# Kernel optimization log

Measured on AMD Instinct MI355X. Metric: run time of the kernel, lower is better.

Reference implementation:

```python
import jax, jax.numpy as jnp
import numpy as np

# Model dims
B, S, H, E, I, K = 2, 2048, 1024, 8, 1024, 2
ALPHA, LIMIT = 1.702, 7.0  # gpt_oss activation constants (module defaults)


def setup_inputs() -> dict:
    key = jax.random.key(0)
    ks = jax.random.split(key, 5)
    sc = 0.02
    return {
        "hidden_states": jax.random.normal(ks[0], (B, S, H), jnp.float32),
        "router_weight": jax.random.normal(ks[1], (H, E), jnp.float32) * sc,
        "gate_up_proj": jax.random.normal(ks[2], (E, H, 2 * I), jnp.float32) * sc,
        "gate_up_proj_bias": jnp.zeros((E, 2 * I), jnp.float32),
        "down_proj": jax.random.normal(ks[3], (E, I, H), jnp.float32) * sc,
        "down_proj_bias": jnp.zeros((E, H), jnp.float32),
    }


def reference(hidden_states, router_weight, gate_up_proj, gate_up_proj_bias,
              down_proj, down_proj_bias):
    Bt, St, Ht = hidden_states.shape
    x = hidden_states.reshape(-1, Ht)           # [T, H], T = B*S
    T = x.shape[0]

    # Router: linear -> top-k -> softmax over selected logits (gpt_oss style)
    logits = x @ router_weight                  # [T, E]
    top_vals, top_idx = jax.lax.top_k(logits, K)
    scores = jax.nn.softmax(top_vals, axis=-1)  # [T, K]
    # Sparse combine weights: w[t, e] = score if e selected for t, else 0
    w = jnp.zeros((T, E), x.dtype).at[jnp.arange(T)[:, None], top_idx].set(scores)

    # Fused gate+up projection for every expert (dense equivalent of grouped GEMM;
    # unselected experts get zero combine weight so math matches sparse path)
    gu = jnp.einsum('th,ehf->tef', x, gate_up_proj) + gate_up_proj_bias  # [T, E, 2I]
    gate = gu[..., ::2]                         # interleaved gate (default)
    up = gu[..., 1::2]
    gate = jnp.minimum(gate, LIMIT)
    up = jnp.clip(up, -LIMIT, LIMIT)
    glu = gate * jax.nn.sigmoid(gate * ALPHA)
    act = (up + 1.0) * glu                      # [T, E, I]

    down = jnp.einsum('tei,eih->teh', act, down_proj) + down_proj_bias  # [T, E, H]

    # Weighted combine over experts (all-to-all combine is identity at D=1)
    out = jnp.einsum('te,teh->th', w, down)     # [T, H]
    return out.reshape(Bt, St, Ht)
```

## Files before the change

kernel.cpp:

```cpp
#include <hip/hip_runtime.h>
#include <hip/hip_bf16.h>
#include <cstdint>
#include <cstddef>

constexpr int T_TOK = 4096;
constexpr int H_DIM = 1024;
constexpr int E_NUM = 8;
constexpr int I_DIM = 1024;
constexpr int F2    = 2048;
constexpr float ALPHA = 1.702f;
constexpr float LIMIT = 7.0f;
constexpr int BM = 128;
constexpr int BK = 32;
constexpr int NT = 32;
constexpr int MAXT = 72;

using u16    = unsigned short;
using bf16x8 = __attribute__((ext_vector_type(8))) __bf16;
using s16x8  = __attribute__((ext_vector_type(8))) short;
using f32x4  = __attribute__((ext_vector_type(4))) float;

constexpr size_t WS_W1T  = 0;
constexpr size_t WS_DOWN = 0;
constexpr size_t WS_W2T  = 33554432;
constexpr size_t WS_ACT  = 50331648;
constexpr size_t WS_ETOK = 67108864;
constexpr size_t WS_POS  = 67239936;
constexpr size_t WS_CNT  = 67272704;
constexpr size_t WS_ROWB = 67272736;
constexpr size_t WS_ASGN = 67272768;
constexpr size_t WS_TOPE = 67273792;
constexpr size_t WS_TOPW = 67290176;
constexpr size_t WS_XBF  = 67322944;
constexpr size_t WS_NEED = 75711552;

__device__ __forceinline__ u16 f2bf(float f) {
    union { float f; unsigned u; } v; v.f = f;
    return (u16)((v.u + 0x7FFFu + ((v.u >> 16) & 1u)) >> 16);
}
__device__ __forceinline__ float bf2f(u16 u) {
    union { unsigned u; float f; } v; v.u = (unsigned)u << 16; return v.f;
}

__device__ __forceinline__ s16x8 pack8(float4 a, float4 b) {
    s16x8 r;
    r[0] = (short)f2bf(a.x); r[1] = (short)f2bf(a.y);
    r[2] = (short)f2bf(a.z); r[3] = (short)f2bf(a.w);
    r[4] = (short)f2bf(b.x); r[5] = (short)f2bf(b.y);
    r[6] = (short)f2bf(b.z); r[7] = (short)f2bf(b.w);
    return r;
}

__device__ __forceinline__ void gload16(const void* g, void* l) {
    __builtin_amdgcn_global_load_lds((const __attribute__((address_space(1))) unsigned*)g,
                                     (__attribute__((address_space(3))) unsigned*)l,
                                     16, 0, 0);
}

__device__ __forceinline__ void pipe_sync() {
    __builtin_amdgcn_sched_barrier(0);
    asm volatile("s_waitcnt vmcnt(0) lgkmcnt(0)" ::: "memory");
    __builtin_amdgcn_s_barrier();
    __builtin_amdgcn_sched_barrier(0);
}

__global__ __launch_bounds__(256) void k_xbf(const float* __restrict__ x,
                                             u16* __restrict__ xbf) {
    const size_t i = ((size_t)blockIdx.x * 256 + threadIdx.x) * 8;
    float4 a = *(const float4*)(x + i);
    float4 b = *(const float4*)(x + i + 4);
    *(s16x8*)(xbf + i) = pack8(a, b);
}

__global__ __launch_bounds__(256) void k_transpose_w1(const float* __restrict__ in,
                                                      u16* __restrict__ out) {
    __shared__ float tile[64][65];
    const int e = blockIdx.z, c0 = blockIdx.x * 64, h0 = blockIdx.y * 64;
    const int tid = threadIdx.x;
    const float* src = in + ((size_t)e * H_DIM + h0) * F2 + c0;
#pragma unroll
    for (int i = 0; i < 4; ++i) {
        int r = (tid >> 4) + i * 16, c = (tid & 15) * 4;
        float4 v = *(const float4*)(src + (size_t)r * F2 + c);
        tile[r][c] = v.x; tile[r][c + 1] = v.y; tile[r][c + 2] = v.z; tile[r][c + 3] = v.w;
    }
    __syncthreads();
    const int c = tid >> 2, hseg = (tid & 3) * 16;
    const int g = c & 1;
    const int f = (c0 + c) >> 1;
    u16* dst = out + (((size_t)e * 2 + g) * I_DIM + f) * H_DIM + h0 + hseg;
    s16x8 o0, o1;
#pragma unroll
    for (int j = 0; j < 8; ++j) o0[j] = (short)f2bf(tile[hseg + j][c]);
#pragma unroll
    for (int j = 0; j < 8; ++j) o1[j] = (short)f2bf(tile[hseg + 8 + j][c]);
    *(s16x8*)dst = o0;
    *(s16x8*)(dst + 8) = o1;
}

__global__ __launch_bounds__(256) void k_transpose_w2(const float* __restrict__ in,
                                                      u16* __restrict__ out) {
    __shared__ float tile[64][65];
    const int e = blockIdx.z, h0 = blockIdx.x * 64, i0 = blockIdx.y * 64;
    const int tid = threadIdx.x;
    const float* src = in + ((size_t)e * I_DIM + i0) * H_DIM + h0;
#pragma unroll
    for (int i = 0; i < 4; ++i) {
        int r = (tid >> 4) + i * 16, c = (tid & 15) * 4;
        float4 v = *(const float4*)(src + (size_t)r * H_DIM + c);
        tile[r][c] = v.x; tile[r][c + 1] = v.y; tile[r][c + 2] = v.z; tile[r][c + 3] = v.w;
    }
    __syncthreads();
    const int c = tid >> 2, iseg = (tid & 3) * 16;
    u16* dst = out + ((size_t)e * H_DIM + h0 + c) * I_DIM + i0 + iseg;
    s16x8 o0, o1;
#pragma unroll
    for (int j = 0; j < 8; ++j) o0[j] = (short)f2bf(tile[iseg + j][c]);
#pragma unroll
    for (int j = 0; j < 8; ++j) o1[j] = (short)f2bf(tile[iseg + 8 + j][c]);
    *(s16x8*)dst = o0;
    *(s16x8*)(dst + 8) = o1;
}

__global__ __launch_bounds__(256) void k_router_top2(const float* __restrict__ x,
                                                     const float* __restrict__ rw,
                                                     int* __restrict__ tope,
                                                     float2* __restrict__ topw) {
    const int wave = threadIdx.x >> 6, lane = threadIdx.x & 63;
    const int t = blockIdx.x * 4 + wave;
    const float* xr = x + (size_t)t * H_DIM;
    float acc[E_NUM];
#pragma unroll
    for (int e = 0; e < E_NUM; ++e) acc[e] = 0.f;
    for (int h = lane; h < H_DIM; h += 64) {
        float xv = xr[h];
        const float* r = rw + h * E_NUM;
#pragma unroll
        for (int e = 0; e < E_NUM; ++e) acc[e] += xv * r[e];
    }
#pragma unroll
    for (int e = 0; e < E_NUM; ++e) {
        float v = acc[e];
#pragma unroll
        for (int o = 32; o > 0; o >>= 1) v += __shfl_down(v, o);
        acc[e] = v;
    }
    if (lane == 0) {
        int e0 = 0; float v0 = acc[0];
#pragma unroll
        for (int e = 1; e < E_NUM; ++e) if (acc[e] > v0) { v0 = acc[e]; e0 = e; }
        int e1 = -1; float v1 = -3.4e38f;
#pragma unroll
        for (int e = 0; e < E_NUM; ++e) if (e != e0 && acc[e] > v1) { v1 = acc[e]; e1 = e; }
        float ew = expf(v1 - v0);
        float inv = 1.f / (1.f + ew);
        tope[t] = e0 | (e1 << 8);
        topw[t] = make_float2(inv, ew * inv);
    }
}

__global__ __launch_bounds__(256) void k_router_scatter(const int* __restrict__ tope,
                                                        int* __restrict__ cnt,
                                                        int* __restrict__ ent_tok,
                                                        int2* __restrict__ pos) {
    __shared__ int lcnt[E_NUM];
    __shared__ int gbase[E_NUM];
    const int tid = threadIdx.x;
    const int t = blockIdx.x * 256 + tid;
    if (tid < E_NUM) lcnt[tid] = 0;
    __syncthreads();
    const int pk = tope[t];
    const int e0 = pk & 0xff, e1 = pk >> 8;
    const int o0 = atomicAdd(&lcnt[e0], 1);
    const int o1 = atomicAdd(&lcnt[e1], 1);
    __syncthreads();
    if (tid < E_NUM) gbase[tid] = atomicAdd(&cnt[tid], lcnt[tid]);
    __syncthreads();
    const int p0 = gbase[e0] + o0;
    const int p1 = gbase[e1] + o1;
    ent_tok[e0 * T_TOK + p0] = t;
    ent_tok[e1 * T_TOK + p1] = t;
    pos[t] = make_int2(p0, p1);
}

__global__ void k_schedule(const int* __restrict__ cnt, int* __restrict__ rowbase,
                           int* __restrict__ assign) {
    if (threadIdx.x == 0) {
        int rb = 0, na = 0;
        for (int e = 0; e < E_NUM; ++e) {
            rowbase[e] = rb;
            int nt = (cnt[e] + BM - 1) >> 7;
            for (int m = 0; m < nt; ++m) assign[na++] = (e << 16) | m;
            rb += cnt[e];
        }
        for (; na < MAXT; ++na) assign[na] = -1;
    }
}

__global__ __launch_bounds__(256, 3) void k_gemm1(
    const u16* __restrict__ xbf, const u16* __restrict__ w1t,
    const float* __restrict__ bias, const int* __restrict__ ent_tok,
    const int* __restrict__ cnt, const int* __restrict__ rowbase,
    const int* __restrict__ assign, u16* __restrict__ act) {
    const int a = assign[blockIdx.y];
    if (a < 0) return;
    const int e = a >> 16, mt = a & 0xffff;
    const int j0 = blockIdx.x * 64;
    const int cs = cnt[e], r0 = mt * BM;
    __shared__ __align__(16) u16 As[2][BM * BK];
    __shared__ __align__(16) u16 Bs[2][BM * BK];
    const int tid = threadIdx.x, lane = tid & 63, wv = tid >> 6;
    const int lr = lane >> 2;
    const int sm = (lane & 3) ^ (lr & 3);
    const u16* asrc[2]; const u16* bsrc[2]; int dofs[2];
#pragma unroll
    for (int j = 0; j < 2; ++j) {
        const int row = wv * 32 + j * 16 + lr;
        const int aent = r0 + row;
        const int tok = (aent < cs) ? ent_tok[e * T_TOK + aent] : 0;
        asrc[j] = xbf + (size_t)tok * H_DIM + sm * 8;
        const int g = row >> 6;
        const int f = j0 + (row & 63);
        bsrc[j] = w1t + (((size_t)e * 2 + g) * I_DIM + f) * H_DIM + sm * 8;
        dofs[j] = (wv * 32 + j * 16) * BK;
    }
    const int wm = wv >> 1, wn = wv & 1;
    const int lcol = lane & 15, lk = lane >> 4;
    int aoff[4], goff[2], uoff[2];
#pragma unroll
    for (int mi = 0; mi < 4; ++mi) {
        const int r = wm * 64 + mi * 16 + lcol;
        aoff[mi] = r * 64 + ((lk ^ (r & 3)) << 4);
    }
#pragma unroll
    for (int nj = 0; nj < 2; ++nj) {
        const int rg_ = wn * 32 + nj * 16 + lcol;
        const int ru  = 64 + rg_;
        goff[nj] = rg_ * 64 + ((lk ^ (rg_ & 3)) << 4);
        uoff[nj] = ru  * 64 + ((lk ^ (ru  & 3)) << 4);
    }
    f32x4 ag[4][2], au[4][2];
    const f32x4 z = {0.f, 0.f, 0.f, 0.f};
#pragma unroll
    for (int mi = 0; mi < 4; ++mi) { ag[mi][0] = z; ag[mi][1] = z; au[mi][0] = z; au[mi][1] = z; }
#pragma unroll
    for (int j = 0; j < 2; ++j) {
        gload16(asrc[j], &As[0][dofs[j]]);
        gload16(bsrc[j], &Bs[0][dofs[j]]);
    }
    pipe_sync();
    int cur = 0;
    for (int t = 0; t < NT; ++t) {
        if (t + 1 < NT) {
            const int kn = (t + 1) * BK;
            u16* Ad = As[cur ^ 1]; u16* Bd = Bs[cur ^ 1];
#pragma unroll
            for (int j = 0; j < 2; ++j) {
                gload16(asrc[j] + kn, Ad + dofs[j]);
                gload16(bsrc[j] + kn, Bd + dofs[j]);
            }
        }
        const char* Ab = (const char*)As[cur];
        const char* Bb = (const char*)Bs[cur];
        bf16x8 af[4];
#pragma unroll
        for (int mi = 0; mi < 4; ++mi) af[mi] = *(const bf16x8*)(Ab + aoff[mi]);
        const bf16x8 g0 = *(const bf16x8*)(Bb + goff[0]);
        const bf16x8 g1 = *(const bf16x8*)(Bb + goff[1]);
        const bf16x8 u0 = *(const bf16x8*)(Bb + uoff[0]);
        const bf16x8 u1 = *(const bf16x8*)(Bb + uoff[1]);
#pragma unroll
        for (int mi = 0; mi < 4; ++mi) {
            ag[mi][0] = __builtin_amdgcn_mfma_f32_16x16x32_bf16(af[mi], g0, ag[mi][0], 0, 0, 0);
            au[mi][0] = __builtin_amdgcn_mfma_f32_16x16x32_bf16(af[mi], u0, au[mi][0], 0, 0, 0);
            ag[mi][1] = __builtin_amdgcn_mfma_f32_16x16x32_bf16(af[mi], g1, ag[mi][1], 0, 0, 0);
            au[mi][1] = __builtin_amdgcn_mfma_f32_16x16x32_bf16(af[mi], u1, au[mi][1], 0, 0, 0);
        }
        pipe_sync();
        cur ^= 1;
    }
    const int rbase = rowbase[e];
#pragma unroll
    for (int mi = 0; mi < 4; ++mi) {
#pragma unroll
        for (int nj = 0; nj < 2; ++nj) {
            const int col = j0 + wn * 32 + nj * 16 + lcol;
            const float bg_ = bias[e * F2 + 2 * col];
            const float bu_ = bias[e * F2 + 2 * col + 1];
#pragma unroll
            for (int rg = 0; rg < 4; ++rg) {
                const int r = wm * 64 + mi * 16 + lk * 4 + rg;
                if (r0 + r < cs) {
                    float gv = ag[mi][nj][rg] + bg_;
                    float uv = au[mi][nj][rg] + bu_;
                    gv = fminf(gv, LIMIT);
                    uv = fminf(fmaxf(uv, -LIMIT), LIMIT);
                    const float glu = gv / (1.f + expf(-ALPHA * gv));
                    act[(size_t)(rbase + r0 + r) * I_DIM + col] = f2bf((uv + 1.f) * glu);
                }
            }
        }
    }
}

__global__ __launch_bounds__(256, 3) void k_gemm2(
    const u16* __restrict__ act, const u16* __restrict__ w2t,
    const int* __restrict__ cnt, const int* __restrict__ rowbase,
    const int* __restrict__ assign, u16* __restrict__ down) {
    const int a = assign[blockIdx.y];
    if (a < 0) return;
    const int e = a >> 16, mt = a & 0xffff;
    const int n0 = blockIdx.x * 128;
    const int cs = cnt[e], r0 = mt * BM, rbase = rowbase[e];
    __shared__ __align__(16) u16 As[2][BM * BK];
    __shared__ __align__(16) u16 Bs[2][BM * BK];
    const int tid = threadIdx.x, lane = tid & 63, wv = tid >> 6;
    const int lr = lane >> 2;
    const int sm = (lane & 3) ^ (lr & 3);
    const u16* asrc[2]; const u16* bsrc[2]; int dofs[2];
#pragma unroll
    for (int j = 0; j < 2; ++j) {
        const int row = wv * 32 + j * 16 + lr;
        int ar = rbase + r0 + row;
        if (ar > 2 * T_TOK - 1) ar = 2 * T_TOK - 1;
        asrc[j] = act + (size_t)ar * I_DIM + sm * 8;
        bsrc[j] = w2t + ((size_t)e * H_DIM + n0 + row) * I_DIM + sm * 8;
        dofs[j] = (wv * 32 + j * 16) * BK;
    }
    const int wm = wv >> 1, wn = wv & 1;
    const int lcol = lane & 15, lk = lane >> 4;
    int aoff[4], boff[4];
#pragma unroll
    for (int mi = 0; mi < 4; ++mi) {
        const int r = wm * 64 + mi * 16 + lcol;
        const int b = wn * 64 + mi * 16 + lcol;
        aoff[mi] = r * 64 + ((lk ^ (r & 3)) << 4);
        boff[mi] = b * 64 + ((lk ^ (b & 3)) << 4);
    }
    f32x4 acc[4][4];
    const f32x4 z = {0.f, 0.f, 0.f, 0.f};
#pragma unroll
    for (int mi = 0; mi < 4; ++mi)
#pragma unroll
        for (int nj = 0; nj < 4; ++nj) acc[mi][nj] = z;
#pragma unroll
    for (int j = 0; j < 2; ++j) {
        gload16(asrc[j], &As[0][dofs[j]]);
        gload16(bsrc[j], &Bs[0][dofs[j]]);
    }
    pipe_sync();
    int cur = 0;
    for (int t = 0; t < NT; ++t) {
        if (t + 1 < NT) {
            const int kn = (t + 1) * BK;
            u16* Ad = As[cur ^ 1]; u16* Bd = Bs[cur ^ 1];
#pragma unroll
            for (int j = 0; j < 2; ++j) {
                gload16(asrc[j] + kn, Ad + dofs[j]);
                gload16(bsrc[j] + kn, Bd + dofs[j]);
            }
        }
        const char* Ab = (const char*)As[cur];
        const char* Bb = (const char*)Bs[cur];
        bf16x8 af[4], bf_[4];
#pragma unroll
        for (int mi = 0; mi < 4; ++mi) af[mi]  = *(const bf16x8*)(Ab + aoff[mi]);
#pragma unroll
        for (int nj = 0; nj < 4; ++nj) bf_[nj] = *(const bf16x8*)(Bb + boff[nj]);
#pragma unroll
        for (int mi = 0; mi < 4; ++mi)
#pragma unroll
            for (int nj = 0; nj < 4; ++nj)
                acc[mi][nj] = __builtin_amdgcn_mfma_f32_16x16x32_bf16(af[mi], bf_[nj], acc[mi][nj], 0, 0, 0);
        pipe_sync();
        cur ^= 1;
    }
#pragma unroll
    for (int mi = 0; mi < 4; ++mi) {
#pragma unroll
        for (int nj = 0; nj < 4; ++nj) {
            const int col = n0 + wn * 64 + nj * 16 + lcol;
#pragma unroll
            for (int rg = 0; rg < 4; ++rg) {
                const int r = wm * 64 + mi * 16 + lk * 4 + rg;
                if (r0 + r < cs)
                    down[(size_t)(rbase + r0 + r) * H_DIM + col] = f2bf(acc[mi][nj][rg]);
            }
        }
    }
}

__global__ __launch_bounds__(256) void k_combine(
    const int* __restrict__ tope, const float2* __restrict__ topw,
    const int2* __restrict__ pos, const int* __restrict__ rowb,
    const float* __restrict__ b2, const u16* __restrict__ down,
    float* __restrict__ out) {
    const int t = blockIdx.x;
    const int c = threadIdx.x * 4;
    const int pk = tope[t];
    const int e0 = pk & 0xff, e1 = pk >> 8;
    const int2 pp = pos[t];
    const float2 w = topw[t];
    const size_t ro0 = (size_t)(rowb[e0] + pp.x) * H_DIM;
    const size_t ro1 = (size_t)(rowb[e1] + pp.y) * H_DIM;
    ushort4 d0 = *(const ushort4*)(down + ro0 + c);
    ushort4 d1 = *(const ushort4*)(down + ro1 + c);
    float4 bb0 = *(const float4*)(b2 + e0 * H_DIM + c);
    float4 bb1 = *(const float4*)(b2 + e1 * H_DIM + c);
    float4 o;
    o.x = w.x * (bf2f(d0.x) + bb0.x) + w.y * (bf2f(d1.x) + bb1.x);
    o.y = w.x * (bf2f(d0.y) + bb0.y) + w.y * (bf2f(d1.y) + bb1.y);
    o.z = w.x * (bf2f(d0.z) + bb0.z) + w.y * (bf2f(d1.z) + bb1.z);
    o.w = w.x * (bf2f(d0.w) + bb0.w) + w.y * (bf2f(d1.w) + bb1.w);
    *(float4*)(out + (size_t)t * H_DIM + c) = o;
}

extern "C" void kernel_launch(void* const* d_in, const int* in_sizes, int n_in,
                              void* d_out, int out_size, void* d_ws, size_t ws_size,
                              hipStream_t stream) {
    const float* x   = (const float*)d_in[0];
    const float* rw  = (const float*)d_in[1];
    const float* w1  = (const float*)d_in[2];
    const float* b1  = (const float*)d_in[3];
    const float* w2  = (const float*)d_in[4];
    const float* b2  = (const float*)d_in[5];
    float* out = (float*)d_out;
    char* ws = (char*)d_ws;

    if (ws_size < WS_NEED) return;

    u16*    W1T  = (u16*)(ws + WS_W1T);
    u16*    DOWN = (u16*)(ws + WS_DOWN);
    u16*    W2T  = (u16*)(ws + WS_W2T);
    u16*    ACT  = (u16*)(ws + WS_ACT);
    int*    ETOK = (int*)(ws + WS_ETOK);
    int2*   POS  = (int2*)(ws + WS_POS);
    int*    CNT  = (int*)(ws + WS_CNT);
    int*    ROWB = (int*)(ws + WS_ROWB);
    int*    ASGN = (int*)(ws + WS_ASGN);
    int*    TOPE = (int*)(ws + WS_TOPE);
    float2* TOPW = (float2*)(ws + WS_TOPW);
    u16*    XBF  = (u16*)(ws + WS_XBF);

    hipMemsetAsync(CNT, 0, E_NUM * sizeof(int), stream);

    k_xbf<<<T_TOK * H_DIM / 2048, 256, 0, stream>>>(x, XBF);
    k_transpose_w1<<<dim3(32, 16, 8), 256, 0, stream>>>(w1, W1T);
    k_transpose_w2<<<dim3(16, 16, 8), 256, 0, stream>>>(w2, W2T);
    k_router_top2<<<T_TOK / 4, 256, 0, stream>>>(x, rw, TOPE, TOPW);
    k_router_scatter<<<T_TOK / 256, 256, 0, stream>>>(TOPE, CNT, ETOK, POS);
    k_schedule<<<1, 64, 0, stream>>>(CNT, ROWB, ASGN);
    k_gemm1<<<dim3(16, MAXT), 256, 0, stream>>>(XBF, W1T, b1, ETOK, CNT, ROWB, ASGN, ACT);
    k_gemm2<<<dim3(8, MAXT), 256, 0, stream>>>(ACT, W2T, CNT, ROWB, ASGN, DOWN);
    k_combine<<<T_TOK, 256, 0, stream>>>(TOPE, TOPW, POS, ROWB, b2, DOWN, out);
}
```

Measured before the change: 166.6 us.

## Restructure MoE GEMMs as persistent 512-thread kernels with triple-buffered 256x64 tiles

Both grouped expert GEMMs become persistent kernels: 256 blocks of 512 threads loop over a job list built from a device-side tile count, replacing the old grid padded with empty tiles. Tiles grow to 256 rows with BK=64 and a three-stage LDS ring, using partial vmcnt waits so loads run two stages ahead of the MFMAs. The LDS swizzle is widened to 8 chunks and s_setprio is raised around the MFMA blocks. The larger tiles and extra LDS buffer reduce occupancy and add more row padding for experts with few tokens.

```diff
diff --git a/kernel.cpp b/kernel.cpp
--- a/kernel.cpp
+++ b/kernel.cpp
@@ -10,10 +10,14 @@
 constexpr int F2    = 2048;
 constexpr float ALPHA = 1.702f;
 constexpr float LIMIT = 7.0f;
-constexpr int BM = 128;
-constexpr int BK = 32;
-constexpr int NT = 32;
-constexpr int MAXT = 72;
+constexpr int BM  = 256;
+constexpr int BK  = 64;
+constexpr int NKT = 16;
+constexpr int BN1 = 64;
+constexpr int NP1 = I_DIM / BN1;
+constexpr int BN2 = 128;
+constexpr int NP2 = H_DIM / BN2;
+constexpr int MAXT = 40;
 
 using u16    = unsigned short;
 using bf16x8 = __attribute__((ext_vector_type(8))) __bf16;
@@ -57,12 +61,9 @@
                                      16, 0, 0);
 }
 
-__device__ __forceinline__ void pipe_sync() {
-    __builtin_amdgcn_sched_barrier(0);
-    asm volatile("s_waitcnt vmcnt(0) lgkmcnt(0)" ::: "memory");
-    __builtin_amdgcn_s_barrier();
-    __builtin_amdgcn_sched_barrier(0);
-}
+#define SB0() __builtin_amdgcn_sched_barrier(0)
+#define BARRIER() do { SB0(); __builtin_amdgcn_s_barrier(); SB0(); } while (0)
+#define WVM(n) asm volatile("s_waitcnt vmcnt(" #n ")" ::: "memory")
 
 __global__ __launch_bounds__(256) void k_xbf(const float* __restrict__ x,
                                              u16* __restrict__ xbf) {
@@ -184,207 +185,252 @@
 }
 
 __global__ void k_schedule(const int* __restrict__ cnt, int* __restrict__ rowbase,
-                           int* __restrict__ assign) {
+                           int* __restrict__ assign, int* __restrict__ ntot) {
     if (threadIdx.x == 0) {
         int rb = 0, na = 0;
         for (int e = 0; e < E_NUM; ++e) {
             rowbase[e] = rb;
-            int nt = (cnt[e] + BM - 1) >> 7;
+            int nt = (cnt[e] + BM - 1) >> 8;
             for (int m = 0; m < nt; ++m) assign[na++] = (e << 16) | m;
             rb += cnt[e];
         }
+        ntot[0] = na;
         for (; na < MAXT; ++na) assign[na] = -1;
     }
 }
 
-__global__ __launch_bounds__(256, 3) void k_gemm1(
+__global__ __launch_bounds__(512, 2) void k_gemm1(
     const u16* __restrict__ xbf, const u16* __restrict__ w1t,
     const float* __restrict__ bias, const int* __restrict__ ent_tok,
     const int* __restrict__ cnt, const int* __restrict__ rowbase,
-    const int* __restrict__ assign, u16* __restrict__ act) {
-    const int a = assign[blockIdx.y];
-    if (a < 0) return;
-    const int e = a >> 16, mt = a & 0xffff;
-    const int j0 = blockIdx.x * 64;
-    const int cs = cnt[e], r0 = mt * BM;
-    __shared__ __align__(16) u16 As[2][BM * BK];
-    __shared__ __align__(16) u16 Bs[2][BM * BK];
+    const int* __restrict__ assign, const int* __restrict__ ntotp,
+    u16* __restrict__ act) {
+    __shared__ __align__(16) u16 As[3][BM * BK];
+    __shared__ __align__(16) u16 Bs[3][128 * BK];
+    const int ntot = ntotp[0];
     const int tid = threadIdx.x, lane = tid & 63, wv = tid >> 6;
-    const int lr = lane >> 2;
-    const int sm = (lane & 3) ^ (lr & 3);
-    const u16* asrc[2]; const u16* bsrc[2]; int dofs[2];
-#pragma unroll
-    for (int j = 0; j < 2; ++j) {
-        const int row = wv * 32 + j * 16 + lr;
-        const int aent = r0 + row;
-        const int tok = (aent < cs) ? ent_tok[e * T_TOK + aent] : 0;
-        asrc[j] = xbf + (size_t)tok * H_DIM + sm * 8;
-        const int g = row >> 6;
-        const int f = j0 + (row & 63);
-        bsrc[j] = w1t + (((size_t)e * 2 + g) * I_DIM + f) * H_DIM + sm * 8;
-        dofs[j] = (wv * 32 + j * 16) * BK;
-    }
+    const int lr8 = lane >> 3;
+    const int sg  = (lane & 7) ^ lr8;
     const int wm = wv >> 1, wn = wv & 1;
     const int lcol = lane & 15, lk = lane >> 4;
-    int aoff[4], goff[2], uoff[2];
+    int aoff[4][2], goff[2][2], uoff[2][2];
 #pragma unroll
     for (int mi = 0; mi < 4; ++mi) {
         const int r = wm * 64 + mi * 16 + lcol;
-        aoff[mi] = r * 64 + ((lk ^ (r & 3)) << 4);
-    }
-#pragma unroll
-    for (int nj = 0; nj < 2; ++nj) {
-        const int rg_ = wn * 32 + nj * 16 + lcol;
-        const int ru  = 64 + rg_;
-        goff[nj] = rg_ * 64 + ((lk ^ (rg_ & 3)) << 4);
-        uoff[nj] = ru  * 64 + ((lk ^ (ru  & 3)) << 4);
-    }
-    f32x4 ag[4][2], au[4][2];
-    const f32x4 z = {0.f, 0.f, 0.f, 0.f};
-#pragma unroll
-    for (int mi = 0; mi < 4; ++mi) { ag[mi][0] = z; ag[mi][1] = z; au[mi][0] = z; au[mi][1] = z; }
-#pragma unroll
-    for (int j = 0; j < 2; ++j) {
-        gload16(asrc[j], &As[0][dofs[j]]);
-        gload16(bsrc[j], &Bs[0][dofs[j]]);
-    }
-    pipe_sync();
-    int cur = 0;
-    for (int t = 0; t < NT; ++t) {
-        if (t + 1 < NT) {
-            const int kn = (t + 1) * BK;
-            u16* Ad = As[cur ^ 1]; u16* Bd = Bs[cur ^ 1];
-#pragma unroll
-            for (int j = 0; j < 2; ++j) {
-                gload16(asrc[j] + kn, Ad + dofs[j]);
-                gload16(bsrc[j] + kn, Bd + dofs[j]);
+#pragma unroll
+        for (int h = 0; h < 2; ++h)
+            aoff[mi][h] = r * 128 + (((h * 4 + lk) ^ (r & 7)) << 4);
+    }
+#pragma unroll
+    for (int fj = 0; fj < 2; ++fj) {
+        const int rg_ = wn * 64 + fj * 16 + lcol;
+        const int ru  = rg_ + 32;
+#pragma unroll
+        for (int h = 0; h < 2; ++h) {
+            goff[fj][h] = rg_ * 128 + (((h * 4 + lk) ^ (rg_ & 7)) << 4);
+            uoff[fj][h] = ru  * 128 + (((h * 4 + lk) ^ (ru  & 7)) << 4);
+        }
+    }
+    const int adst[4] = { (0 * 64 + wv * 8) * BK, (1 * 64 + wv * 8) * BK,
+                          (2 * 64 + wv * 8) * BK, (3 * 64 + wv * 8) * BK };
+    const int bdst[2] = { (0 * 64 + wv * 8) * BK, (1 * 64 + wv * 8) * BK };
+
+    for (int job = blockIdx.x; job < ntot * NP1; job += gridDim.x) {
+        const int pan = job & (NP1 - 1), ti = job >> 4;
+        const int a = assign[ti];
+        const int e = a >> 16, mt = a & 0xffff;
+        const int j0 = pan * BN1;
+        const int cs = cnt[e], r0 = mt * BM, rbase = rowbase[e];
+        const u16* asrc[4]; const u16* bsrc[2];
+#pragma unroll
+        for (int j = 0; j < 4; ++j) {
+            const int row = j * 64 + wv * 8 + lr8;
+            const int aent = r0 + row;
+            const int tok = (aent < cs) ? ent_tok[e * T_TOK + aent] : 0;
+            asrc[j] = xbf + (size_t)tok * H_DIM + sg * 8;
+        }
+#pragma unroll
+        for (int j = 0; j < 2; ++j) {
+            const int i = wv * 8 + lr8;
+            const int g = (i >= 32);
+            const int col = j0 + j * 32 + (i & 31);
+            bsrc[j] = w1t + (((size_t)e * 2 + g) * I_DIM + col) * H_DIM + sg * 8;
+        }
+        f32x4 ag[4][2], au[4][2];
+        const f32x4 z = {0.f, 0.f, 0.f, 0.f};
+#pragma unroll
+        for (int mi = 0; mi < 4; ++mi) { ag[mi][0] = z; ag[mi][1] = z; au[mi][0] = z; au[mi][1] = z; }
+
+#define G1_STAGE(kt, buf) do {                                              \
+        const int kb_ = (kt) * BK;                                          \
+        _Pragma("unroll") for (int j = 0; j < 4; ++j)                       \
+            gload16(asrc[j] + kb_, &As[buf][adst[j]]);                      \
+        _Pragma("unroll") for (int j = 0; j < 2; ++j)                       \
+            gload16(bsrc[j] + kb_, &Bs[buf][bdst[j]]);                      \
+    } while (0)
+
+        G1_STAGE(0, 0);
+        G1_STAGE(1, 1);
+        int cur = 0;
+        for (int t = 0; t < NKT; ++t) {
+            int nxt = cur + 2; if (nxt >= 3) nxt -= 3;
+            if (t + 2 < NKT) { G1_STAGE(t + 2, nxt); WVM(12); }
+            else if (t + 1 < NKT) { WVM(6); }
+            else { WVM(0); }
+            BARRIER();
+            const char* Ab = (const char*)(&As[cur][0]);
+            const char* Bb = (const char*)(&Bs[cur][0]);
+#pragma unroll
+            for (int h = 0; h < 2; ++h) {
+                bf16x8 af[4], gf[2], uf[2];
+#pragma unroll
+                for (int mi = 0; mi < 4; ++mi) af[mi] = *(const bf16x8*)(Ab + aoff[mi][h]);
+#pragma unroll
+                for (int fj = 0; fj < 2; ++fj) {
+                    gf[fj] = *(const bf16x8*)(Bb + goff[fj][h]);
+                    uf[fj] = *(const bf16x8*)(Bb + uoff[fj][h]);
+                }
+                __builtin_amdgcn_s_setprio(1);
+#pragma unroll
+                for (int mi = 0; mi < 4; ++mi) {
+                    ag[mi][0] = __builtin_amdgcn_mfma_f32_16x16x32_bf16(af[mi], gf[0], ag[mi][0], 0, 0, 0);
+                    au[mi][0] = __builtin_amdgcn_mfma_f32_16x16x32_bf16(af[mi], uf[0], au[mi][0], 0, 0, 0);
+                    ag[mi][1] = __builtin_amdgcn_mfma_f32_16x16x32_bf16(af[mi], gf[1], ag[mi][1], 0, 0, 0);
+                    au[mi][1] = __builtin_amdgcn_mfma_f32_16x16x32_bf16(af[mi], uf[1], au[mi][1], 0, 0, 0);
+                }
+                __builtin_amdgcn_s_setprio(0);
             }
-        }
-        const char* Ab = (const char*)As[cur];
-        const char* Bb = (const char*)Bs[cur];
-        bf16x8 af[4];
-#pragma unroll
-        for (int mi = 0; mi < 4; ++mi) af[mi] = *(const bf16x8*)(Ab + aoff[mi]);
-        const bf16x8 g0 = *(const bf16x8*)(Bb + goff[0]);
-        const bf16x8 g1 = *(const bf16x8*)(Bb + goff[1]);
-        const bf16x8 u0 = *(const bf16x8*)(Bb + uoff[0]);
-        const bf16x8 u1 = *(const bf16x8*)(Bb + uoff[1]);
+            BARRIER();
+            cur = cur + 1; if (cur >= 3) cur -= 3;
+        }
+#undef G1_STAGE
 #pragma unroll
         for (int mi = 0; mi < 4; ++mi) {
-            ag[mi][0] = __builtin_amdgcn_mfma_f32_16x16x32_bf16(af[mi], g0, ag[mi][0], 0, 0, 0);
-            au[mi][0] = __builtin_amdgcn_mfma_f32_16x16x32_bf16(af[mi], u0, au[mi][0], 0, 0, 0);
-            ag[mi][1] = __builtin_amdgcn_mfma_f32_16x16x32_bf16(af[mi], g1, ag[mi][1], 0, 0, 0);
-            au[mi][1] = __builtin_amdgcn_mfma_f32_16x16x32_bf16(af[mi], u1, au[mi][1], 0, 0, 0);
-        }
-        pipe_sync();
-        cur ^= 1;
-    }
-    const int rbase = rowbase[e];
-#pragma unroll
-    for (int mi = 0; mi < 4; ++mi) {
-#pragma unroll
-        for (int nj = 0; nj < 2; ++nj) {
-            const int col = j0 + wn * 32 + nj * 16 + lcol;
-            const float bg_ = bias[e * F2 + 2 * col];
-            const float bu_ = bias[e * F2 + 2 * col + 1];
-#pragma unroll
-            for (int rg = 0; rg < 4; ++rg) {
-                const int r = wm * 64 + mi * 16 + lk * 4 + rg;
-                if (r0 + r < cs) {
-                    float gv = ag[mi][nj][rg] + bg_;
-                    float uv = au[mi][nj][rg] + bu_;
-                    gv = fminf(gv, LIMIT);
-                    uv = fminf(fmaxf(uv, -LIMIT), LIMIT);
-                    const float glu = gv / (1.f + expf(-ALPHA * gv));
-                    act[(size_t)(rbase + r0 + r) * I_DIM + col] = f2bf((uv + 1.f) * glu);
+#pragma unroll
+            for (int fj = 0; fj < 2; ++fj) {
+                const int col = j0 + wn * 32 + fj * 16 + lcol;
+                const float bg_ = bias[e * F2 + 2 * col];
+                const float bu_ = bias[e * F2 + 2 * col + 1];
+#pragma unroll
+                for (int rg = 0; rg < 4; ++rg) {
+                    const int r = wm * 64 + mi * 16 + lk * 4 + rg;
+                    if (r0 + r < cs) {
+                        float gv = ag[mi][fj][rg] + bg_;
+                        float uv = au[mi][fj][rg] + bu_;
+                        gv = fminf(gv, LIMIT);
+                        uv = fminf(fmaxf(uv, -LIMIT), LIMIT);
+                        const float glu = gv / (1.f + expf(-ALPHA * gv));
+                        act[(size_t)(rbase + r0 + r) * I_DIM + col] = f2bf((uv + 1.f) * glu);
+                    }
                 }
             }
         }
     }
 }
 
-__global__ __launch_bounds__(256, 3) void k_gemm2(
+__global__ __launch_bounds__(512, 2) void k_gemm2(
     const u16* __restrict__ act, const u16* __restrict__ w2t,
     const int* __restrict__ cnt, const int* __restrict__ rowbase,
-    const int* __restrict__ assign, u16* __restrict__ down) {
-    const int a = assign[blockIdx.y];
-    if (a < 0) return;
-    const int e = a >> 16, mt = a & 0xffff;
-    const int n0 = blockIdx.x * 128;
-    const int cs = cnt[e], r0 = mt * BM, rbase = rowbase[e];
-    __shared__ __align__(16) u16 As[2][BM * BK];
-    __shared__ __align__(16) u16 Bs[2][BM * BK];
+    const int* __restrict__ assign, const int* __restrict__ ntotp,
+    u16* __restrict__ down) {
+    __shared__ __align__(16) u16 As[3][BM * BK];
+    __shared__ __align__(16) u16 Bs[3][128 * BK];
+    const int ntot = ntotp[0];
     const int tid = threadIdx.x, lane = tid & 63, wv = tid >> 6;
-    const int lr = lane >> 2;
-    const int sm = (lane & 3) ^ (lr & 3);
-    const u16* asrc[2]; const u16* bsrc[2]; int dofs[2];
-#pragma unroll
-    for (int j = 0; j < 2; ++j) {
-        const int row = wv * 32 + j * 16 + lr;
-        int ar = rbase + r0 + row;
-        if (ar > 2 * T_TOK - 1) ar = 2 * T_TOK - 1;
-        asrc[j] = act + (size_t)ar * I_DIM + sm * 8;
-        bsrc[j] = w2t + ((size_t)e * H_DIM + n0 + row) * I_DIM + sm * 8;
-        dofs[j] = (wv * 32 + j * 16) * BK;
-    }
+    const int lr8 = lane >> 3;
+    const int sg  = (lane & 7) ^ lr8;
     const int wm = wv >> 1, wn = wv & 1;
     const int lcol = lane & 15, lk = lane >> 4;
-    int aoff[4], boff[4];
+    int aoff[4][2], boff[4][2];
 #pragma unroll
     for (int mi = 0; mi < 4; ++mi) {
         const int r = wm * 64 + mi * 16 + lcol;
         const int b = wn * 64 + mi * 16 + lcol;
-        aoff[mi] = r * 64 + ((lk ^ (r & 3)) << 4);
-        boff[mi] = b * 64 + ((lk ^ (b & 3)) << 4);
-    }
-    f32x4 acc[4][4];
-    const f32x4 z = {0.f, 0.f, 0.f, 0.f};
-#pragma unroll
-    for (int mi = 0; mi < 4; ++mi)
-#pragma unroll
-        for (int nj = 0; nj < 4; ++nj) acc[mi][nj] = z;
-#pragma unroll
-    for (int j = 0; j < 2; ++j) {
-        gload16(asrc[j], &As[0][dofs[j]]);
-        gload16(bsrc[j], &Bs[0][dofs[j]]);
-    }
-    pipe_sync();
-    int cur = 0;
-    for (int t = 0; t < NT; ++t) {
-        if (t + 1 < NT) {
-            const int kn = (t + 1) * BK;
-            u16* Ad = As[cur ^ 1]; u16* Bd = Bs[cur ^ 1];
-#pragma unroll
-            for (int j = 0; j < 2; ++j) {
-                gload16(asrc[j] + kn, Ad + dofs[j]);
-                gload16(bsrc[j] + kn, Bd + dofs[j]);
+#pragma unroll
+        for (int h = 0; h < 2; ++h) {
+            aoff[mi][h] = r * 128 + (((h * 4 + lk) ^ (r & 7)) << 4);
+            boff[mi][h] = b * 128 + (((h * 4 + lk) ^ (b & 7)) << 4);
+        }
+    }
+    const int adst[4] = { (0 * 64 + wv * 8) * BK, (1 * 64 + wv * 8) * BK,
+                          (2 * 64 + wv * 8) * BK, (3 * 64 + wv * 8) * BK };
+    const int bdst[2] = { (0 * 64 + wv * 8) * BK, (1 * 64 + wv * 8) * BK };
+
+    for (int job = blockIdx.x; job < ntot * NP2; job += gridDim.x) {
+        const int pan = job & (NP2 - 1), ti = job >> 3;
+        const int a = assign[ti];
+        const int e = a >> 16, mt = a & 0xffff;
+        const int n0 = pan * BN2;
+        const int cs = cnt[e], r0 = mt * BM, rbase = rowbase[e];
+        const u16* asrc[4]; const u16* bsrc[2];
+#pragma unroll
+        for (int j = 0; j < 4; ++j) {
+            const int row = j * 64 + wv * 8 + lr8;
+            int ar = rbase + r0 + row;
+            if (ar > 2 * T_TOK - 1) ar = 2 * T_TOK - 1;
+            asrc[j] = act + (size_t)ar * I_DIM + sg * 8;
+        }
+#pragma unroll
+        for (int j = 0; j < 2; ++j) {
+            const int row = j * 64 + wv * 8 + lr8;
+            bsrc[j] = w2t + ((size_t)e * H_DIM + n0 + row) * I_DIM + sg * 8;
+        }
+        f32x4 acc[4][4];
+        const f32x4 z = {0.f, 0.f, 0.f, 0.f};
+#pragma unroll
+        for (int mi = 0; mi < 4; ++mi)
+#pragma unroll
+            for (int nj = 0; nj < 4; ++nj) acc[mi][nj] = z;
+
+#define G2_STAGE(kt, buf) do {                                              \
+        const int kb_ = (kt) * BK;                                          \
+        _Pragma("unroll") for (int j = 0; j < 4; ++j)                       \
+            gload16(asrc[j] + kb_, &As[buf][adst[j]]);                      \
+        _Pragma("unroll") for (int j = 0; j < 2; ++j)                       \
+            gload16(bsrc[j] + kb_, &Bs[buf][bdst[j]]);                      \
+    } while (0)
+
+        G2_STAGE(0, 0);
+        G2_STAGE(1, 1);
+        int cur = 0;
+        for (int t = 0; t < NKT; ++t) {
+            int nxt = cur + 2; if (nxt >= 3) nxt -= 3;
+            if (t + 2 < NKT) { G2_STAGE(t + 2, nxt); WVM(12); }
+            else if (t + 1 < NKT) { WVM(6); }
+            else { WVM(0); }
+            BARRIER();
+            const char* Ab = (const char*)(&As[cur][0]);
+            const char* Bb = (const char*)(&Bs[cur][0]);
+#pragma unroll
+            for (int h = 0; h < 2; ++h) {
+                bf16x8 af[4], bf_[4];
+#pragma unroll
+                for (int mi = 0; mi < 4; ++mi) af[mi]  = *(const bf16x8*)(Ab + aoff[mi][h]);
+#pragma unroll
+                for (int nj = 0; nj < 4; ++nj) bf_[nj] = *(const bf16x8*)(Bb + boff[nj][h]);
+                __builtin_amdgcn_s_setprio(1);
+#pragma unroll
+                for (int mi = 0; mi < 4; ++mi)
+#pragma unroll
+                    for (int nj = 0; nj < 4; ++nj)
+                        acc[mi][nj] = __builtin_amdgcn_mfma_f32_16x16x32_bf16(af[mi], bf_[nj], acc[mi][nj], 0, 0, 0);
+                __builtin_amdgcn_s_setprio(0);
             }
-        }
-        const char* Ab = (const char*)As[cur];
-        const char* Bb = (const char*)Bs[cur];
-        bf16x8 af[4], bf_[4];
-#pragma unroll
-        for (int mi = 0; mi < 4; ++mi) af[mi]  = *(const bf16x8*)(Ab + aoff[mi]);
-#pragma unroll
-        for (int nj = 0; nj < 4; ++nj) bf_[nj] = *(const bf16x8*)(Bb + boff[nj]);
-#pragma unroll
-        for (int mi = 0; mi < 4; ++mi)
-#pragma unroll
-            for (int nj = 0; nj < 4; ++nj)
-                acc[mi][nj] = __builtin_amdgcn_mfma_f32_16x16x32_bf16(af[mi], bf_[nj], acc[mi][nj], 0, 0, 0);
-        pipe_sync();
-        cur ^= 1;
-    }
-#pragma unroll
-    for (int mi = 0; mi < 4; ++mi) {
-#pragma unroll
-        for (int nj = 0; nj < 4; ++nj) {
-            const int col = n0 + wn * 64 + nj * 16 + lcol;
-#pragma unroll
-            for (int rg = 0; rg < 4; ++rg) {
-                const int r = wm * 64 + mi * 16 + lk * 4 + rg;
-                if (r0 + r < cs)
-                    down[(size_t)(rbase + r0 + r) * H_DIM + col] = f2bf(acc[mi][nj][rg]);
+            BARRIER();
+            cur = cur + 1; if (cur >= 3) cur -= 3;
+        }
+#undef G2_STAGE
+#pragma unroll
+        for (int mi = 0; mi < 4; ++mi) {
+#pragma unroll
+            for (int nj = 0; nj < 4; ++nj) {
+                const int col = n0 + wn * 64 + nj * 16 + lcol;
+#pragma unroll
+                for (int rg = 0; rg < 4; ++rg) {
+                    const int r = wm * 64 + mi * 16 + lk * 4 + rg;
+                    if (r0 + r < cs)
+                        down[(size_t)(rbase + r0 + r) * H_DIM + col] = f2bf(acc[mi][nj][rg]);
+                }
             }
         }
     }
@@ -438,6 +484,7 @@
     int*    CNT  = (int*)(ws + WS_CNT);
     int*    ROWB = (int*)(ws + WS_ROWB);
     int*    ASGN = (int*)(ws + WS_ASGN);
+    int*    NTOT = ASGN + MAXT;
     int*    TOPE = (int*)(ws + WS_TOPE);
     float2* TOPW = (float2*)(ws + WS_TOPW);
     u16*    XBF  = (u16*)(ws + WS_XBF);
@@ -449,8 +496,8 @@
     k_transpose_w2<<<dim3(16, 16, 8), 256, 0, stream>>>(w2, W2T);
     k_router_top2<<<T_TOK / 4, 256, 0, stream>>>(x, rw, TOPE, TOPW);
     k_router_scatter<<<T_TOK / 256, 256, 0, stream>>>(TOPE, CNT, ETOK, POS);
-    k_schedule<<<1, 64, 0, stream>>>(CNT, ROWB, ASGN);
-    k_gemm1<<<dim3(16, MAXT), 256, 0, stream>>>(XBF, W1T, b1, ETOK, CNT, ROWB, ASGN, ACT);
-    k_gemm2<<<dim3(8, MAXT), 256, 0, stream>>>(ACT, W2T, CNT, ROWB, ASGN, DOWN);
+    k_schedule<<<1, 64, 0, stream>>>(CNT, ROWB, ASGN, NTOT);
+    k_gemm1<<<256, 512, 0, stream>>>(XBF, W1T, b1, ETOK, CNT, ROWB, ASGN, NTOT, ACT);
+    k_gemm2<<<256, 512, 0, stream>>>(ACT, W2T, CNT, ROWB, ASGN, NTOT, DOWN);
     k_combine<<<T_TOK, 256, 0, stream>>>(TOPE, TOPW, POS, ROWB, b2, DOWN, out);
 }
```

Result: slower. 200.5 us (+20.4%).
